# Kernel tuning notes

Hardware: AMD Instinct MI355X
Metric: run time of the kernel (lower is better)

Reference implementation:

```python
import jax, jax.numpy as jnp
import numpy as np

B, C, HID, NH, HD, NCT = 4096, 16, 1024, 16, 64, 32
SCALE = 8.0  # sqrt(head_dim=64)


def _ln(x, g, b, eps=1e-5):
    m = jnp.mean(x, axis=-1, keepdims=True)
    v = jnp.mean((x - m) ** 2, axis=-1, keepdims=True)
    return (x - m) * jax.lax.rsqrt(v + eps) * g + b


def setup_inputs() -> dict:
    key = jax.random.key(0)
    ks = jax.random.split(key, 16)
    s = 0.02
    w = lambda k, shape: jax.random.normal(k, shape, jnp.float32) * s
    return {
        'channel_tokens': jax.random.normal(ks[0], (B, C, HID), jnp.float32),
        'cancer_type': jax.random.randint(ks[1], (B,), 0, NCT),
        'channel_active': jax.random.randint(ks[2], (B, C), 0, 10) > 0,
        'Wq': w(ks[3], (HID, HID)), 'bq': jnp.zeros((HID,), jnp.float32),
        'Wk': w(ks[4], (HID, HID)), 'bk': jnp.zeros((HID,), jnp.float32),
        'Wv': w(ks[5], (HID, HID)), 'bv': jnp.zeros((HID,), jnp.float32),
        'Wo': w(ks[6], (HID, HID)), 'bo': jnp.zeros((HID,), jnp.float32),
        'ct_bias_emb': w(ks[7], (NCT, C * C)),
        'ct_key_emb': w(ks[8], (NCT, HID)),
        'ln1_g': jnp.ones((HID,), jnp.float32), 'ln1_b': jnp.zeros((HID,), jnp.float32),
        'ln2_g': jnp.ones((HID,), jnp.float32), 'ln2_b': jnp.zeros((HID,), jnp.float32),
        'W1': w(ks[9], (HID, 2 * HID)), 'b1': jnp.zeros((2 * HID,), jnp.float32),
        'W2': w(ks[10], (2 * HID, HID)), 'b2': jnp.zeros((HID,), jnp.float32),
    }


def reference(channel_tokens, cancer_type, channel_active,
              Wq, bq, Wk, bk, Wv, bv, Wo, bo,
              ct_bias_emb, ct_key_emb,
              ln1_g, ln1_b, ln2_g, ln2_b,
              W1, b1, W2, b2):
    x = channel_tokens  # (B, C, HID)
    normed = _ln(x, ln1_g, ln1_b)
    # QKV, split heads: (B, C, NH, HD)
    q = (normed @ Wq + bq).reshape(B, C, NH, HD)
    k = (normed @ Wk + bk).reshape(B, C, NH, HD)
    v = (normed @ Wv + bv).reshape(B, C, NH, HD)
    # cancer-type key modulation: (B, 1, NH, HD), broadcast over channels
    k = k + ct_key_emb[cancer_type].reshape(B, 1, NH, HD)
    # scores (B, NH, C, C)
    attn = jnp.einsum('bqhd,bkhd->bhqk', q, k) / SCALE
    # per-batch cancer-type channel bias
    ct_bias = ct_bias_emb[cancer_type].reshape(B, C, C)
    attn = attn + ct_bias[:, None, :, :] * 0.1
    # mask inactive key channels
    attn = jnp.where(channel_active[:, None, None, :], attn, -jnp.inf)
    p = jnp.nan_to_num(jax.nn.softmax(attn, axis=-1), nan=0.0)
    # dropout is identity in eval mode
    out = jnp.einsum('bhqk,bkhd->bqhd', p, v).reshape(B, C, HID)
    x = x + (out @ Wo + bo)
    h = _ln(x, ln2_g, ln2_b)
    h = jax.nn.elu(h @ W1 + b1) @ W2 + b2
    return x + h
```

## Files before the change

kernel.cpp:

```cpp
#include <hip/hip_runtime.h>
#include <hip/hip_bf16.h>

#define BB   4096
#define CC   16
#define HIDN 1024
#define NHD  16
#define HDIM 64
#define MROWS (BB*CC)
#define QKVN 3072

using u16 = unsigned short;
typedef __bf16 bf16x8 __attribute__((ext_vector_type(8)));
typedef float  f32x4  __attribute__((ext_vector_type(4)));

__device__ __forceinline__ u16 f2b(float f) {
  union { __hip_bfloat16 h; u16 u; } c;
  c.h = __float2bfloat16(f);
  return c.u;
}

__global__ __launch_bounds__(256) void transpose_cast(
    const float* __restrict__ src, u16* __restrict__ dst, int R, int C) {
  __shared__ float tile[32][33];
  const int bx = blockIdx.x * 32;
  const int by = blockIdx.y * 32;
  const int tx = threadIdx.x, ty = threadIdx.y;
#pragma unroll
  for (int jj = 0; jj < 32; jj += 8)
    tile[ty + jj][tx] = src[(long long)(by + ty + jj) * C + bx + tx];
  __syncthreads();
#pragma unroll
  for (int jj = 0; jj < 32; jj += 8)
    dst[(long long)(bx + ty + jj) * R + by + tx] = f2b(tile[tx][ty + jj]);
}

__global__ __launch_bounds__(256) void ln_kernel(
    const float* __restrict__ x, const float* __restrict__ g,
    const float* __restrict__ b, u16* __restrict__ out) {
  const int row = blockIdx.x;
  const int t = threadIdx.x;
  const float4 v = ((const float4*)(x + (long long)row * HIDN))[t];
  float s  = v.x + v.y + v.z + v.w;
  float sq = v.x * v.x + v.y * v.y + v.z * v.z + v.w * v.w;
#pragma unroll
  for (int off = 32; off; off >>= 1) {
    s  += __shfl_down(s, off);
    sq += __shfl_down(sq, off);
  }
  __shared__ float ws[8];
  const int w = t >> 6, lane = t & 63;
  if (lane == 0) { ws[w] = s; ws[4 + w] = sq; }
  __syncthreads();
  const float S  = ws[0] + ws[1] + ws[2] + ws[3];
  const float SQ = ws[4] + ws[5] + ws[6] + ws[7];
  const float mean = S * (1.f / HIDN);
  const float var  = SQ * (1.f / HIDN) - mean * mean;
  const float rstd = rsqrtf(var + 1e-5f);
  const float4 gg = ((const float4*)g)[t];
  const float4 bb = ((const float4*)b)[t];
  ushort4 o;
  o.x = f2b((v.x - mean) * rstd * gg.x + bb.x);
  o.y = f2b((v.y - mean) * rstd * gg.y + bb.y);
  o.z = f2b((v.z - mean) * rstd * gg.z + bb.z);
  o.w = f2b((v.w - mean) * rstd * gg.w + bb.w);
  ((ushort4*)(out + (long long)row * HIDN))[t] = o;
}

#define BM 128
#define BN 128
#define BK 64

template <int EPI>
__global__ __launch_bounds__(256, 2) void gemm_bt(
    const u16* __restrict__ A, const u16* __restrict__ BT, int K,
    const float* __restrict__ bias, const float* __restrict__ bias2,
    const float* __restrict__ bias3, const float* __restrict__ resid,
    const int* __restrict__ ctype, const float* __restrict__ ct_key,
    float* __restrict__ outF, u16* __restrict__ outB, int N) {
  __shared__ u16 As[BM * BK];
  __shared__ u16 Bs[BN * BK];

  const int t = threadIdx.x;
  const int lane = t & 63;
  const int w = t >> 6;
  const int wm = w & 1, wn = w >> 1;
  const int lane15 = lane & 15;
  const int quad = lane >> 4;
  const int nblk = blockIdx.x, mblk = blockIdx.y;

  const long long Abase = (long long)mblk * BM * K;
  const long long Bbase = (long long)nblk * BN * K;

  f32x4 acc[4][4] = {};

  for (int kk = 0; kk < K; kk += BK) {
#pragma unroll
    for (int j = 0; j < 4; ++j) {
      const int c = j * 256 + t;
      const int row = c >> 3;
      const int kcs = c & 7;
      const int kct = kcs ^ (row & 7);
      const u16* gA = A + Abase + (long long)row * K + kk + kct * 8;
      const u16* gB = BT + Bbase + (long long)row * K + kk + kct * 8;
      __builtin_amdgcn_global_load_lds(
          (const __attribute__((address_space(1))) void*)gA,
          (__attribute__((address_space(3))) void*)(As + c * 8), 16, 0, 0);
      __builtin_amdgcn_global_load_lds(
          (const __attribute__((address_space(1))) void*)gB,
          (__attribute__((address_space(3))) void*)(Bs + c * 8), 16, 0, 0);
    }
    __syncthreads();

#pragma unroll
    for (int k0 = 0; k0 < 2; ++k0) {
      const int kc = k0 * 4 + quad;
      bf16x8 af[4], bfr[4];
#pragma unroll
      for (int im = 0; im < 4; ++im) {
        const int m = wm * 64 + im * 16 + lane15;
        af[im] = *(const bf16x8*)(As + (m * 8 + (kc ^ (m & 7))) * 8);
      }
#pragma unroll
      for (int in = 0; in < 4; ++in) {
        const int n = wn * 64 + in * 16 + lane15;
        bfr[in] = *(const bf16x8*)(Bs + (n * 8 + (kc ^ (n & 7))) * 8);
      }
#pragma unroll
      for (int im = 0; im < 4; ++im)
#pragma unroll
        for (int in = 0; in < 4; ++in)
          acc[im][in] = __builtin_amdgcn_mfma_f32_16x16x32_bf16(
              af[im], bfr[in], acc[im][in], 0, 0, 0);
    }
    __syncthreads();
  }

  const int rowBase = mblk * BM + wm * 64 + quad * 4;
  const int colBase = nblk * BN + wn * 64 + lane15;

  const float* bsel = bias;
  bool addct = false;
  if constexpr (EPI == 1) {
    const int sub = nblk >> 3;
    bsel = (sub == 0) ? bias : (sub == 1 ? bias2 : bias3);
    addct = (sub == 1);
  }

#pragma unroll
  for (int in = 0; in < 4; ++in) {
    const int col = colBase + in * 16;
    float bv;
    if constexpr (EPI == 1) {
      bv = bsel[col & 1023];
    } else {
      bv = bias[col];
    }
#pragma unroll
    for (int im = 0; im < 4; ++im) {
#pragma unroll
      for (int r = 0; r < 4; ++r) {
        const int row = rowBase + im * 16 + r;
        float v = acc[im][in][r] + bv;
        const long long oidx = (long long)row * N + col;
        if constexpr (EPI == 1) {
          if (addct) v += ct_key[(long long)ctype[row >> 4] * HIDN + (col & 1023)];
          outB[oidx] = f2b(v);
        } else if constexpr (EPI == 2) {
          outF[oidx] = v + resid[oidx];
        } else if constexpr (EPI == 3) {
          v = v > 0.f ? v : __expf(v) - 1.f;
          outB[oidx] = f2b(v);
        } else {
          outB[oidx] = f2b(v);
        }
      }
    }
  }
}

__global__ __launch_bounds__(256) void attn_kernel(
    const u16* __restrict__ QKV, const int* __restrict__ cancer_type,
    const int* __restrict__ channel_active,
    const float* __restrict__ ct_bias_emb, u16* __restrict__ out) {
  __shared__ u16 Ks[CC * HIDN];
  __shared__ u16 Vs[CC * HIDN];
  const int b = blockIdx.x;
  const int t = threadIdx.x;

#pragma unroll
  for (int j = 0; j < 8; ++j) {
    const int c = j * 256 + t;
    const int row = c >> 7;
    const int off = c & 127;
    const long long base = (long long)(b * CC + row) * QKVN;
    ((float4*)Ks)[c] = *(const float4*)(QKV + base + 1024 + off * 8);
    ((float4*)Vs)[c] = *(const float4*)(QKV + base + 2048 + off * 8);
  }
  __syncthreads();

  const int h = t >> 4, i = t & 15;
  const int ct = cancer_type[b];
  const float* ctb = ct_bias_emb + ct * (CC * CC) + i * CC;

  float q[HDIM];
  const u16* qg = QKV + ((long long)(b * CC + i) * QKVN + h * HDIM);
#pragma unroll
  for (int c = 0; c < 8; ++c) {
    const bf16x8 v = *(const bf16x8*)(qg + c * 8);
#pragma unroll
    for (int e = 0; e < 8; ++e) q[c * 8 + e] = (float)v[e];
  }

  float s[CC];
#pragma unroll
  for (int j = 0; j < CC; ++j) {
    const u16* kr = Ks + j * HIDN + h * HDIM;
    float a = 0.f;
#pragma unroll
    for (int c = 0; c < 8; ++c) {
      const bf16x8 kv = *(const bf16x8*)(kr + c * 8);
#pragma unroll
      for (int e = 0; e < 8; ++e) a += q[c * 8 + e] * (float)kv[e];
    }
    a = a * 0.125f + 0.1f * ctb[j];
    if (channel_active[b * CC + j] == 0) a = -__builtin_inff();
    s[j] = a;
  }

  float mx = -__builtin_inff();
#pragma unroll
  for (int j = 0; j < CC; ++j) mx = fmaxf(mx, s[j]);
  float p[CC];
  float sum = 0.f;
  const bool dead = (mx == -__builtin_inff());
#pragma unroll
  for (int j = 0; j < CC; ++j) {
    p[j] = dead ? 0.f : __expf(s[j] - mx);
    sum += p[j];
  }
  const float inv = sum > 0.f ? 1.f / sum : 0.f;

  float o[HDIM] = {};
#pragma unroll
  for (int j = 0; j < CC; ++j) {
    const float pw = p[j] * inv;
    const u16* vr = Vs + j * HIDN + h * HDIM;
#pragma unroll
    for (int c = 0; c < 8; ++c) {
      const bf16x8 vv = *(const bf16x8*)(vr + c * 8);
#pragma unroll
      for (int e = 0; e < 8; ++e) o[c * 8 + e] += pw * (float)vv[e];
    }
  }

  u16* og = out + ((long long)(b * CC + i) * HIDN + h * HDIM);
#pragma unroll
  for (int c = 0; c < 8; ++c) {
    uint4 u;
    u.x = (unsigned)f2b(o[c * 8 + 0]) | ((unsigned)f2b(o[c * 8 + 1]) << 16);
    u.y = (unsigned)f2b(o[c * 8 + 2]) | ((unsigned)f2b(o[c * 8 + 3]) << 16);
    u.z = (unsigned)f2b(o[c * 8 + 4]) | ((unsigned)f2b(o[c * 8 + 5]) << 16);
    u.w = (unsigned)f2b(o[c * 8 + 6]) | ((unsigned)f2b(o[c * 8 + 7]) << 16);
    ((uint4*)og)[c] = u;
  }
}

extern "C" void kernel_launch(void* const* d_in, const int* in_sizes, int n_in,
                              void* d_out, int out_size, void* d_ws,
                              size_t ws_size, hipStream_t stream) {
  const float* x            = (const float*)d_in[0];
  const int*   cancer_type  = (const int*)d_in[1];
  const int*   channel_act  = (const int*)d_in[2];
  const float* Wq = (const float*)d_in[3];  const float* bq = (const float*)d_in[4];
  const float* Wk = (const float*)d_in[5];  const float* bk = (const float*)d_in[6];
  const float* Wv = (const float*)d_in[7];  const float* bv = (const float*)d_in[8];
  const float* Wo = (const float*)d_in[9];  const float* bo = (const float*)d_in[10];
  const float* ct_bias_emb = (const float*)d_in[11];
  const float* ct_key_emb  = (const float*)d_in[12];
  const float* ln1_g = (const float*)d_in[13]; const float* ln1_b = (const float*)d_in[14];
  const float* ln2_g = (const float*)d_in[15]; const float* ln2_b = (const float*)d_in[16];
  const float* W1 = (const float*)d_in[17]; const float* b1 = (const float*)d_in[18];
  const float* W2 = (const float*)d_in[19]; const float* b2 = (const float*)d_in[20];
  float* out = (float*)d_out;

  u16* WqkvT = (u16*)d_ws;
  u16* WoT = WqkvT + (size_t)QKVN * 1024;
  u16* W1T = WoT + (size_t)1024 * 1024;
  u16* W2T = W1T + (size_t)2048 * 1024;
  u16* normed = W2T + (size_t)1024 * 2048;
  u16* QKV = normed + (size_t)MROWS * HIDN;
  u16* attnO = normed;
  u16* h2    = QKV;
  u16* act   = QKV + (size_t)MROWS * HIDN;
  float* x2  = (float*)d_out;

  const dim3 tb(32, 8);
  transpose_cast<<<dim3(32, 32), tb, 0, stream>>>(Wq, WqkvT, 1024, 1024);
  transpose_cast<<<dim3(32, 32), tb, 0, stream>>>(Wk, WqkvT + (size_t)1024 * 1024, 1024, 1024);
  transpose_cast<<<dim3(32, 32), tb, 0, stream>>>(Wv, WqkvT + (size_t)2048 * 1024, 1024, 1024);
  transpose_cast<<<dim3(32, 32), tb, 0, stream>>>(Wo, WoT, 1024, 1024);
  transpose_cast<<<dim3(64, 32), tb, 0, stream>>>(W1, W1T, 1024, 2048);
  transpose_cast<<<dim3(32, 64), tb, 0, stream>>>(W2, W2T, 2048, 1024);

  ln_kernel<<<MROWS, 256, 0, stream>>>(x, ln1_g, ln1_b, normed);

  gemm_bt<1><<<dim3(24, 512), 256, 0, stream>>>(
      normed, WqkvT, 1024, bq, bk, bv, nullptr, cancer_type, ct_key_emb,
      nullptr, QKV, QKVN);

  attn_kernel<<<BB, 256, 0, stream>>>(QKV, cancer_type, channel_act,
                                      ct_bias_emb, attnO);

  gemm_bt<2><<<dim3(8, 512), 256, 0, stream>>>(
      attnO, WoT, 1024, bo, nullptr, nullptr, x, nullptr, nullptr,
      x2, nullptr, 1024);

  ln_kernel<<<MROWS, 256, 0, stream>>>(x2, ln2_g, ln2_b, h2);

  gemm_bt<3><<<dim3(16, 512), 256, 0, stream>>>(
      h2, W1T, 1024, b1, nullptr, nullptr, nullptr, nullptr, nullptr,
      nullptr, act, 2048);

  gemm_bt<2><<<dim3(8, 512), 256, 0, stream>>>(
      act, W2T, 2048, b2, nullptr, nullptr, x2, nullptr, nullptr,
      out, nullptr, 1024);
}
```

Measured before the change: 2.423 ms.

## Replace GEMM with 256x256 double-buffered, 8-wave pipelined kernel and XCD-aware block remap

Replaces the 128x128 single-buffered bf16 GEMM with a 256x256 tile kernel that uses 512 threads and double-buffered LDS. Global-to-LDS loads for the next K tile are interleaved with MFMA quadrant computation, using explicit vmcnt waits, barriers and s_setprio. It also remaps workgroup IDs so consecutive tiles are spread across chiplets (flat&7 swizzle). The aim is better data reuse and latency hiding, at the cost of 128KB of LDS per block and more registers, which may limit occupancy.

```diff
diff --git a/kernel.cpp b/kernel.cpp
--- a/kernel.cpp
+++ b/kernel.cpp
@@ -66,112 +66,191 @@
   ((ushort4*)(out + (long long)row * HIDN))[t] = o;
 }
 
-#define BM 128
-#define BN 128
-#define BK 64
+#define TBM 256
+#define TBN 256
+#define TBK 64
 
 template <int EPI>
-__global__ __launch_bounds__(256, 2) void gemm_bt(
+__global__ __launch_bounds__(512, 2) void gemm256(
     const u16* __restrict__ A, const u16* __restrict__ BT, int K,
     const float* __restrict__ bias, const float* __restrict__ bias2,
     const float* __restrict__ bias3, const float* __restrict__ resid,
     const int* __restrict__ ctype, const float* __restrict__ ct_key,
     float* __restrict__ outF, u16* __restrict__ outB, int N) {
-  __shared__ u16 As[BM * BK];
-  __shared__ u16 Bs[BN * BK];
+  __shared__ __align__(16) u16 smem[2][2][TBM * TBK];
 
   const int t = threadIdx.x;
   const int lane = t & 63;
   const int w = t >> 6;
-  const int wm = w & 1, wn = w >> 1;
-  const int lane15 = lane & 15;
+  const int l15 = lane & 15;
   const int quad = lane >> 4;
-  const int nblk = blockIdx.x, mblk = blockIdx.y;
-
-  const long long Abase = (long long)mblk * BM * K;
-  const long long Bbase = (long long)nblk * BN * K;
-
-  f32x4 acc[4][4] = {};
-
-  for (int kk = 0; kk < K; kk += BK) {
-#pragma unroll
-    for (int j = 0; j < 4; ++j) {
-      const int c = j * 256 + t;
-      const int row = c >> 3;
-      const int kcs = c & 7;
-      const int kct = kcs ^ (row & 7);
-      const u16* gA = A + Abase + (long long)row * K + kk + kct * 8;
-      const u16* gB = BT + Bbase + (long long)row * K + kk + kct * 8;
-      __builtin_amdgcn_global_load_lds(
-          (const __attribute__((address_space(1))) void*)gA,
-          (__attribute__((address_space(3))) void*)(As + c * 8), 16, 0, 0);
-      __builtin_amdgcn_global_load_lds(
-          (const __attribute__((address_space(1))) void*)gB,
-          (__attribute__((address_space(3))) void*)(Bs + c * 8), 16, 0, 0);
-    }
-    __syncthreads();
-
-#pragma unroll
-    for (int k0 = 0; k0 < 2; ++k0) {
-      const int kc = k0 * 4 + quad;
-      bf16x8 af[4], bfr[4];
-#pragma unroll
-      for (int im = 0; im < 4; ++im) {
-        const int m = wm * 64 + im * 16 + lane15;
-        af[im] = *(const bf16x8*)(As + (m * 8 + (kc ^ (m & 7))) * 8);
-      }
-#pragma unroll
-      for (int in = 0; in < 4; ++in) {
-        const int n = wn * 64 + in * 16 + lane15;
-        bfr[in] = *(const bf16x8*)(Bs + (n * 8 + (kc ^ (n & 7))) * 8);
-      }
-#pragma unroll
-      for (int im = 0; im < 4; ++im)
-#pragma unroll
-        for (int in = 0; in < 4; ++in)
-          acc[im][in] = __builtin_amdgcn_mfma_f32_16x16x32_bf16(
-              af[im], bfr[in], acc[im][in], 0, 0, 0);
-    }
-    __syncthreads();
-  }
-
-  const int rowBase = mblk * BM + wm * 64 + quad * 4;
-  const int colBase = nblk * BN + wn * 64 + lane15;
+  const int wrow = w >> 2;
+  const int wcol = w & 3;
+
+  const int gx = gridDim.x;
+  const int nwg = gx * (int)gridDim.y;
+  const int flat = (int)blockIdx.y * gx + (int)blockIdx.x;
+  const int logical = (flat & 7) * (nwg >> 3) + (flat >> 3);
+  const int nblk = logical % gx;
+  const int mblk = logical / gx;
+
+  const long long Abase = (long long)mblk * TBM * K;
+  const long long Bbase = (long long)nblk * TBN * K;
+
+  #define STAGE(buf, mat, h, kk, base, gp)                                       \
+  do {                                                                           \
+    _Pragma("unroll") for (int s_ = 0; s_ < 2; ++s_) {                           \
+      const int idx_ = (h) * 1024 + (w * 2 + s_) * 64 + lane;                    \
+      const int row_ = idx_ >> 3;                                                \
+      const int kc_ = (idx_ & 7) ^ (row_ & 7);                                   \
+      const u16* g_ = (gp) + (base) + (long long)row_ * K + (kk) + kc_ * 8;      \
+      __builtin_amdgcn_global_load_lds(                                          \
+          (const __attribute__((address_space(1))) void*)g_,                     \
+          (__attribute__((address_space(3))) void*)(&smem[buf][mat][idx_ * 8]),  \
+          16, 0, 0);                                                             \
+    }                                                                            \
+  } while (0)
+
+  bf16x8 aR[4][2];
+  bf16x8 bR[2][2];
+
+  #define RDA(cb, i)                                                             \
+  do {                                                                           \
+    _Pragma("unroll") for (int fm_ = 0; fm_ < 4; ++fm_) {                        \
+      const int row_ = (i) * 128 + wrow * 64 + fm_ * 16 + l15;                   \
+      _Pragma("unroll") for (int ks_ = 0; ks_ < 2; ++ks_) {                      \
+        const int kc_ = ks_ * 4 + quad;                                          \
+        aR[fm_][ks_] = *(const bf16x8*)(                                         \
+            &smem[cb][0][(row_ * 8 + (kc_ ^ (row_ & 7))) * 8]);                  \
+      }                                                                          \
+    }                                                                            \
+  } while (0)
+
+  #define RDB(cb, j)                                                             \
+  do {                                                                           \
+    _Pragma("unroll") for (int fn_ = 0; fn_ < 2; ++fn_) {                        \
+      const int row_ = (j) * 128 + wcol * 32 + fn_ * 16 + l15;                   \
+      _Pragma("unroll") for (int ks_ = 0; ks_ < 2; ++ks_) {                      \
+        const int kc_ = ks_ * 4 + quad;                                          \
+        bR[fn_][ks_] = *(const bf16x8*)(                                         \
+            &smem[cb][1][(row_ * 8 + (kc_ ^ (row_ & 7))) * 8]);                  \
+      }                                                                          \
+    }                                                                            \
+  } while (0)
+
+  f32x4 acc[2][2][4][2] = {};
+
+  #define MM(i, j)                                                               \
+  do {                                                                           \
+    __builtin_amdgcn_s_setprio(1);                                               \
+    _Pragma("unroll") for (int fm_ = 0; fm_ < 4; ++fm_)                          \
+      _Pragma("unroll") for (int fn_ = 0; fn_ < 2; ++fn_)                        \
+        _Pragma("unroll") for (int ks_ = 0; ks_ < 2; ++ks_)                      \
+          acc[i][j][fm_][fn_] = __builtin_amdgcn_mfma_f32_16x16x32_bf16(         \
+              aR[fm_][ks_], bR[fn_][ks_], acc[i][j][fm_][fn_], 0, 0, 0);         \
+    __builtin_amdgcn_s_setprio(0);                                               \
+  } while (0)
+
+  #define WAITV(n) asm volatile("s_waitcnt vmcnt(" #n ")" ::: "memory")
+  #define BAR() __builtin_amdgcn_s_barrier()
+
+  STAGE(0, 0, 0, 0, Abase, A);
+  STAGE(0, 1, 0, 0, Bbase, BT);
+  STAGE(0, 1, 1, 0, Bbase, BT);
+  STAGE(0, 0, 1, 0, Abase, A);
+  WAITV(4);
+  BAR();
+
+  const int NT = K >> 6;
+  for (int tt = 0; tt < NT - 1; ++tt) {
+    const int cb = tt & 1, nb = cb ^ 1;
+    const int kk = (tt + 1) << 6;
+    RDA(cb, 0); RDB(cb, 0);
+    STAGE(nb, 0, 0, kk, Abase, A);
+    STAGE(nb, 1, 0, kk, Bbase, BT);
+    WAITV(6); BAR();
+    MM(0, 0);
+    BAR();
+    RDB(cb, 1);
+    STAGE(nb, 1, 1, kk, Bbase, BT);
+    WAITV(6); BAR();
+    MM(0, 1);
+    BAR();
+    RDA(cb, 1);
+    STAGE(nb, 0, 1, kk, Abase, A);
+    BAR();
+    MM(1, 1);
+    BAR();
+    RDB(cb, 0);
+    WAITV(4); BAR();
+    MM(1, 0);
+    BAR();
+  }
+  {
+    const int cb = (NT - 1) & 1;
+    RDA(cb, 0); RDB(cb, 0);
+    WAITV(2); BAR();
+    MM(0, 0);
+    BAR();
+    RDB(cb, 1);
+    WAITV(0); BAR();
+    MM(0, 1);
+    BAR();
+    RDA(cb, 1);
+    MM(1, 1);
+    RDB(cb, 0);
+    MM(1, 0);
+  }
+
+  #undef STAGE
+  #undef RDA
+  #undef RDB
+  #undef MM
+  #undef WAITV
+  #undef BAR
 
   const float* bsel = bias;
   bool addct = false;
   if constexpr (EPI == 1) {
-    const int sub = nblk >> 3;
+    const int sub = nblk >> 2;
     bsel = (sub == 0) ? bias : (sub == 1 ? bias2 : bias3);
     addct = (sub == 1);
   }
 
 #pragma unroll
-  for (int in = 0; in < 4; ++in) {
-    const int col = colBase + in * 16;
-    float bv;
-    if constexpr (EPI == 1) {
-      bv = bsel[col & 1023];
-    } else {
-      bv = bias[col];
-    }
-#pragma unroll
-    for (int im = 0; im < 4; ++im) {
-#pragma unroll
-      for (int r = 0; r < 4; ++r) {
-        const int row = rowBase + im * 16 + r;
-        float v = acc[im][in][r] + bv;
-        const long long oidx = (long long)row * N + col;
+  for (int i = 0; i < 2; ++i) {
+#pragma unroll
+    for (int j = 0; j < 2; ++j) {
+#pragma unroll
+      for (int fn = 0; fn < 2; ++fn) {
+        const int col = nblk * TBN + j * 128 + wcol * 32 + fn * 16 + l15;
+        float bv;
         if constexpr (EPI == 1) {
-          if (addct) v += ct_key[(long long)ctype[row >> 4] * HIDN + (col & 1023)];
-          outB[oidx] = f2b(v);
-        } else if constexpr (EPI == 2) {
-          outF[oidx] = v + resid[oidx];
-        } else if constexpr (EPI == 3) {
-          v = v > 0.f ? v : __expf(v) - 1.f;
-          outB[oidx] = f2b(v);
+          bv = bsel[col & 1023];
         } else {
-          outB[oidx] = f2b(v);
+          bv = bias[col];
+        }
+#pragma unroll
+        for (int fm = 0; fm < 4; ++fm) {
+#pragma unroll
+          for (int r = 0; r < 4; ++r) {
+            const int row =
+                mblk * TBM + i * 128 + wrow * 64 + fm * 16 + quad * 4 + r;
+            float v = acc[i][j][fm][fn][r] + bv;
+            const long long oidx = (long long)row * N + col;
+            if constexpr (EPI == 1) {
+              if (addct)
+                v += ct_key[(long long)ctype[row >> 4] * HIDN + (col & 1023)];
+              outB[oidx] = f2b(v);
+            } else if constexpr (EPI == 2) {
+              outF[oidx] = v + resid[oidx];
+            } else if constexpr (EPI == 3) {
+              v = v > 0.f ? v : __expf(v) - 1.f;
+              outB[oidx] = f2b(v);
+            } else {
+              outB[oidx] = f2b(v);
+            }
+          }
         }
       }
     }
@@ -304,24 +383,24 @@
 
   ln_kernel<<<MROWS, 256, 0, stream>>>(x, ln1_g, ln1_b, normed);
 
-  gemm_bt<1><<<dim3(24, 512), 256, 0, stream>>>(
+  gemm256<1><<<dim3(12, 256), 512, 0, stream>>>(
       normed, WqkvT, 1024, bq, bk, bv, nullptr, cancer_type, ct_key_emb,
       nullptr, QKV, QKVN);
 
   attn_kernel<<<BB, 256, 0, stream>>>(QKV, cancer_type, channel_act,
                                       ct_bias_emb, attnO);
 
-  gemm_bt<2><<<dim3(8, 512), 256, 0, stream>>>(
+  gemm256<2><<<dim3(4, 256), 512, 0, stream>>>(
       attnO, WoT, 1024, bo, nullptr, nullptr, x, nullptr, nullptr,
       x2, nullptr, 1024);
 
   ln_kernel<<<MROWS, 256, 0, stream>>>(x2, ln2_g, ln2_b, h2);
 
-  gemm_bt<3><<<dim3(16, 512), 256, 0, stream>>>(
+  gemm256<3><<<dim3(8, 256), 512, 0, stream>>>(
       h2, W1T, 1024, b1, nullptr, nullptr, nullptr, nullptr, nullptr,
       nullptr, act, 2048);
 
-  gemm_bt<2><<<dim3(8, 512), 256, 0, stream>>>(
+  gemm256<2><<<dim3(4, 256), 512, 0, stream>>>(
       act, W2T, 2048, b2, nullptr, nullptr, x2, nullptr, nullptr,
       out, nullptr, 1024);
 }
```

Result: faster. 2.099 ms (-13.4%).
